# Optimization experiments

Measured on AMD Instinct MI355X. Metric: run time of the kernel, lower is better.

## Reference

```python
import jax, jax.numpy as jnp
import numpy as np
import math

B, S, D, H = 4, 1024, 1024, 16
Dh = D // H
THETA = 10000.0
LAMBDA_INIT = 0.8  # current_lambda_init_for_scaling (no set_lambda_init_for_scaling call)
GN_EPS = 1e-5


def setup_inputs() -> dict:
    key = jax.random.key(0)
    ks = jax.random.split(key, 14)
    w = 0.02
    return {
        "x_norm": jax.random.normal(ks[0], (B, S, D), jnp.float32),
        "learned_lambda": jax.random.uniform(ks[1], (), jnp.float32),
        "hierarchical_mask_C": jax.random.uniform(ks[2], (1, 1, S, S), jnp.float32),
        "padding_mask": jnp.ones((B, S), jnp.int32),
        "wq_w": jax.random.normal(ks[3], (2 * D, D), jnp.float32) * w,
        "wq_b": jnp.zeros((2 * D,), jnp.float32),
        "wk_w": jax.random.normal(ks[4], (2 * D, D), jnp.float32) * w,
        "wk_b": jnp.zeros((2 * D,), jnp.float32),
        "wv_w": jax.random.normal(ks[5], (D, D), jnp.float32) * w,
        "wv_b": jnp.zeros((D,), jnp.float32),
        "out_w": jax.random.normal(ks[6], (D, D), jnp.float32) * w,
        "out_b": jnp.zeros((D,), jnp.float32),
        "gn_w": jnp.ones((D,), jnp.float32),
        "gn_b": jnp.zeros((D,), jnp.float32),
    }


def _rope_tables(seq_len):
    freqs = 1.0 / (THETA ** (jnp.arange(0, Dh, 2, dtype=jnp.float32) / Dh))  # [Dh/2]
    t = jnp.arange(seq_len, dtype=jnp.float32)
    ang = jnp.outer(t, freqs)  # [S, Dh/2]
    return jnp.cos(ang), jnp.sin(ang)


def _apply_rope(x, cos, sin):
    # x: [B,H,S,Dh]; cos/sin: [S,Dh/2] broadcast over B,H
    x1, x2 = x[..., : Dh // 2], x[..., Dh // 2 :]
    return jnp.concatenate((x1 * cos - x2 * sin, x1 * sin + x2 * cos), axis=-1)


def _heads(x):
    # [B,S,D] -> [B,H,S,Dh]
    b, s, _ = x.shape
    return x.reshape(b, s, H, Dh).transpose(0, 2, 1, 3)


def _masked_softmax(q, k, key_pad_bad):
    scores = jnp.einsum("bhqd,bhkd->bhqk", q, k) / math.sqrt(Dh)
    scores = jnp.where(key_pad_bad[:, None, None, :], -1e9, scores)
    return jax.nn.softmax(scores, axis=-1)


def reference(x_norm, learned_lambda, hierarchical_mask_C, padding_mask,
              wq_w, wq_b, wk_w, wk_b, wv_w, wv_b, out_w, out_b, gn_w, gn_b):
    b, s, _ = x_norm.shape
    q_proj = x_norm @ wq_w.T + wq_b  # [B,S,2D]
    k_proj = x_norm @ wk_w.T + wk_b
    v_proj = x_norm @ wv_w.T + wv_b
    q1, q2 = _heads(q_proj[..., :D]), _heads(q_proj[..., D:])
    k1, k2 = _heads(k_proj[..., :D]), _heads(k_proj[..., D:])
    v = _heads(v_proj)

    cos, sin = _rope_tables(s)
    q1, k1 = _apply_rope(q1, cos, sin), _apply_rope(k1, cos, sin)
    q2, k2 = _apply_rope(q2, cos, sin), _apply_rope(k2, cos, sin)

    key_pad_bad = padding_mask == 0  # [B,S]
    a1 = _masked_softmax(q1, k1, key_pad_bad)
    a2 = _masked_softmax(q2, k2, key_pad_bad)
    diff = a1 - learned_lambda * a2
    combined = hierarchical_mask_C * diff  # [B,H,S,S]

    ctx = jnp.einsum("bhqk,bhkd->bhqd", combined, v)  # [B,H,S,Dh]
    merged = ctx.transpose(0, 2, 1, 3).reshape(b, s, D)  # [B,S,D]

    # GroupNorm(n_heads, d_model) applied on [B, D, S]: normalize per (batch, head-group)
    g = merged.reshape(b, s, H, Dh)
    mean = g.mean(axis=(1, 3), keepdims=True)
    var = ((g - mean) ** 2).mean(axis=(1, 3), keepdims=True)
    normed = ((g - mean) * jax.lax.rsqrt(var + GN_EPS)).reshape(b, s, D)
    normed = normed * gn_w + gn_b

    scaled = normed * (1.0 - LAMBDA_INIT)
    output = scaled @ out_w.T + out_b
    return output, a1, a2
```

## Files before the change

kernel.cpp:

```cpp
#include <hip/hip_runtime.h>
#include <hip/hip_bf16.h>
#include <hip/hip_fp16.h>
#include <cstdint>

#define HSZ    4194304ull
#define S_LEN  1024
#define NHEAD  16
#define DH     64

typedef __attribute__((ext_vector_type(8))) short bf16x8;
typedef __attribute__((ext_vector_type(8))) unsigned short u16x8;
typedef __attribute__((ext_vector_type(4))) unsigned short u16x4;
typedef __attribute__((ext_vector_type(4))) float f32x4;
#define MFMA(a,b,c) __builtin_amdgcn_mfma_f32_16x16x32_bf16(a,b,c,0,0,0)

__device__ __forceinline__ unsigned short f2bf(float f) {
    union { float f; uint32_t u; } v; v.f = f;
    uint32_t r = (v.u + 0x7fffu + ((v.u >> 16) & 1u)) >> 16;
    return (unsigned short)r;
}
__device__ __forceinline__ float bf2f(unsigned short u) {
    union { uint32_t u; float f; } v; v.u = (uint32_t)u << 16;
    return v.f;
}
__device__ __forceinline__ unsigned short f2h(float f) { return __half_as_ushort(__float2half(f)); }
__device__ __forceinline__ float h2f(unsigned short u) { return __half2float(__ushort_as_half(u)); }

__device__ __forceinline__ void bar_lds() {
    asm volatile("s_waitcnt lgkmcnt(0)" ::: "memory");
    __builtin_amdgcn_s_barrier();
}

__global__ __launch_bounds__(256) void conv_x_kernel(
    const float* __restrict__ X, unsigned short* __restrict__ xh, unsigned short* __restrict__ xl)
{
    const int idx = blockIdx.x * 256 + threadIdx.x;
    float4 a = *(const float4*)&X[idx * 8];
    float4 b = *(const float4*)&X[idx * 8 + 4];
    float v[8] = {a.x, a.y, a.z, a.w, b.x, b.y, b.z, b.w};
    u16x8 hi, lo;
#pragma unroll
    for (int j = 0; j < 8; ++j) {
        unsigned short h = f2bf(v[j]);
        hi[j] = h;
        lo[j] = f2bf(v[j] - bf2f(h));
    }
    *(u16x8*)&xh[idx * 8] = hi;
    *(u16x8*)&xl[idx * 8] = lo;
}

__global__ __launch_bounds__(256) void conv_w_kernel(
    const float* __restrict__ wq, const float* __restrict__ wk,
    const float* __restrict__ wv, const float* __restrict__ wo,
    unsigned short* __restrict__ Wcat)
{
    const int idx = blockIdx.x * 256 + threadIdx.x;
    const int row = idx >> 7;
    const int cg  = idx & 127;
    const float* src;
    int rl;
    if (row < 2048)      { src = wq; rl = row; }
    else if (row < 4096) { src = wk; rl = row - 2048; }
    else if (row < 5120) { src = wv; rl = row - 4096; }
    else                 { src = wo; rl = row - 5120; }
    float4 a = *(const float4*)&src[(size_t)rl * 1024 + cg * 8];
    float4 b = *(const float4*)&src[(size_t)rl * 1024 + cg * 8 + 4];
    float v[8] = {a.x, a.y, a.z, a.w, b.x, b.y, b.z, b.w};
    u16x8 o;
#pragma unroll
    for (int j = 0; j < 8; ++j) o[j] = f2bf(v[j]);
    *(u16x8*)&Wcat[(size_t)row * 1024 + cg * 8] = o;
}

__global__ __launch_bounds__(256) void conv_c_kernel(
    const float* __restrict__ C, unsigned short* __restrict__ Cb)
{
    const int idx = blockIdx.x * 256 + threadIdx.x;
    float4 a = *(const float4*)&C[idx * 8];
    float4 b = *(const float4*)&C[idx * 8 + 4];
    float v[8] = {a.x, a.y, a.z, a.w, b.x, b.y, b.z, b.w};
    u16x8 o;
#pragma unroll
    for (int j = 0; j < 8; ++j) o[j] = f2bf(v[j]);
    *(u16x8*)&Cb[idx * 8] = o;
}

__global__ __launch_bounds__(256) void proj_mfma_kernel(
    const unsigned short* __restrict__ xh, const unsigned short* __restrict__ xl,
    const unsigned short* __restrict__ Wcat,
    const float* __restrict__ bq, const float* __restrict__ bk, const float* __restrict__ bv,
    unsigned short* __restrict__ qk, unsigned short* __restrict__ vt)
{
    __shared__ __align__(16) unsigned short Ah[128 * 64];
    __shared__ __align__(16) unsigned short Al[128 * 64];
    __shared__ __align__(16) unsigned short Bs[128 * 64];

    const int t   = threadIdx.x;
    const int bid = blockIdx.x;
    const int swz = (bid & 7) * 160 + (bid >> 3);
    const int n_idx = swz % 40, m_idx = swz / 40;
    const int m0 = m_idx * 128, n0 = n_idx * 128;
    const int w = t >> 6, l = t & 63, ln = l & 15, kg = l >> 4;
    const int wm = w >> 1, wn = w & 1;
    const bool useLo = (n0 < 2048);

    f32x4 acc[4][4];
#pragma unroll
    for (int i = 0; i < 4; ++i)
#pragma unroll
        for (int j = 0; j < 4; ++j) acc[i][j] = (f32x4){0.f, 0.f, 0.f, 0.f};

    for (int k0 = 0; k0 < 1024; k0 += 64) {
        __syncthreads();
#pragma unroll
        for (int i = 0; i < 4; ++i) {
            const int e   = t + i * 256;
            const int row = e >> 3, cg = e & 7;
            const int off = (row * 128 + cg * 16) ^ ((row & 7) << 4);
            const size_t ga = (size_t)(m0 + row) * 1024 + k0 + cg * 8;
            const size_t gb = (size_t)(n0 + row) * 1024 + k0 + cg * 8;
            *(bf16x8*)((char*)Ah + off) = *(const bf16x8*)(xh + ga);
            if (useLo)
                *(bf16x8*)((char*)Al + off) = *(const bf16x8*)(xl + ga);
            *(bf16x8*)((char*)Bs + off) = *(const bf16x8*)(Wcat + gb);
        }
        __syncthreads();
#pragma unroll
        for (int ks = 0; ks < 2; ++ks) {
            bf16x8 bfrag[4];
#pragma unroll
            for (int nj = 0; nj < 4; ++nj) {
                const int row = wn * 64 + nj * 16 + ln;
                const int off = (row * 128 + ks * 64 + kg * 16) ^ ((row & 7) << 4);
                bfrag[nj] = *(const bf16x8*)((const char*)Bs + off);
            }
#pragma unroll
            for (int mi = 0; mi < 4; ++mi) {
                const int row = wm * 64 + mi * 16 + ln;
                const int off = (row * 128 + ks * 64 + kg * 16) ^ ((row & 7) << 4);
                bf16x8 ah = *(const bf16x8*)((const char*)Ah + off);
#pragma unroll
                for (int nj = 0; nj < 4; ++nj)
                    acc[mi][nj] = MFMA(ah, bfrag[nj], acc[mi][nj]);
                if (useLo) {
                    bf16x8 al = *(const bf16x8*)((const char*)Al + off);
#pragma unroll
                    for (int nj = 0; nj < 4; ++nj)
                        acc[mi][nj] = MFMA(al, bfrag[nj], acc[mi][nj]);
                }
            }
        }
    }

    const int seg = (n0 < 2048) ? 0 : (n0 < 4096 ? 1 : 2);
    if (seg < 2) {
        const float* bias = (seg == 0) ? bq : bk;
#pragma unroll
        for (int njp = 0; njp < 2; ++njp) {
            const int n1  = n0 + wn * 64 + njp * 16 + ln;
            const int nl1 = n1 - seg * 2048;
            const int head = (nl1 >> 6) & 15;
            const int dd   = nl1 & 63;
            const float bb1 = bias[nl1];
            const float bb2 = bias[nl1 + 32];
            const float freq = exp2f((float)dd * (-13.287712379549449f / 32.0f));
            unsigned short* hiT;
            unsigned short* loT = nullptr;
            if (seg == 0) {
                const int tq = (nl1 >> 10);
                hiT = qk + (size_t)(tq * 2)     * HSZ;
                loT = qk + (size_t)(tq * 2 + 1) * HSZ;
            } else {
                hiT = qk + (size_t)(4 + (nl1 >> 10)) * HSZ;
            }
#pragma unroll
            for (int mi = 0; mi < 4; ++mi) {
                const int mb = m0 + wm * 64 + mi * 16 + kg * 4;
#pragma unroll
                for (int r = 0; r < 4; ++r) {
                    const int m = mb + r, b_ = m >> 10, s = m & 1023;
                    float sn, cs;
                    sincosf((float)s * freq, &sn, &cs);
                    const float x1 = acc[mi][njp][r]     + bb1;
                    const float x2 = acc[mi][njp + 2][r] + bb2;
                    const float r1 = x1 * cs - x2 * sn;
                    const float r2 = x1 * sn + x2 * cs;
                    const size_t base = (((size_t)(b_ * 16 + head)) * 1024 + s) * 64;
                    const unsigned short h1 = f2bf(r1), h2 = f2bf(r2);
                    hiT[base + dd]      = h1;
                    hiT[base + dd + 32] = h2;
                    if (seg == 0) {
                        loT[base + dd]      = f2bf(r1 - bf2f(h1));
                        loT[base + dd + 32] = f2bf(r2 - bf2f(h2));
                    }
                }
            }
        }
    } else {
#pragma unroll
        for (int mi = 0; mi < 4; ++mi) {
#pragma unroll
            for (int nj = 0; nj < 4; ++nj) {
                const int n  = n0 + wn * 64 + nj * 16 + ln;
                const int nl = n - 4096;
                const float bb = bv[nl];
                const int head = nl >> 6, d = nl & 63;
                const int mb = m0 + wm * 64 + mi * 16 + kg * 4;
                const int b = mb >> 10, sb = mb & 1023;
                u16x4 o;
#pragma unroll
                for (int r = 0; r < 4; ++r) o[r] = f2bf(acc[mi][nj][r] + bb);
                *(u16x4*)(vt + ((size_t)(b * 16 + head) * 64 + d) * 1024 + sb) = o;
            }
        }
    }
}

__global__ __launch_bounds__(512, 4) void attn_kernel(
    const unsigned short* __restrict__ qk,
    const unsigned short* __restrict__ vt,
    const unsigned short* __restrict__ Cb,
    const int* __restrict__ pad,
    const float* __restrict__ lam_p,
    float* __restrict__ out_a1, float* __restrict__ out_a2,
    float* __restrict__ merged)
{
    __shared__ __align__(16) unsigned short sc[16][1032];
    __shared__ __align__(16) float pmax[16][8];
    __shared__ __align__(16) f32x4 red[256];

    const int t  = threadIdx.x;
    const int w  = t >> 6;
    const int l  = t & 63;
    const int ln = l & 15;
    const int g  = l >> 4;
    const int kf = g * 8;

    const int flat = blockIdx.x;
    const int virt = (flat & 7) * 512 + (flat >> 3);
    const int bh = virt >> 6, b = bh >> 4, h = bh & 15;
    const int q0 = (virt & 63) * 16;
    const float lam = lam_p[0];

    const f32x4 Z = {0.f, 0.f, 0.f, 0.f};
    f32x4 ctx = Z;
    const int dt  = w & 3;
    const int khf = w >> 2;

    uint32_t padm = 0;
#pragma unroll
    for (int j = 0; j < 8; ++j)
        padm |= (pad[b * S_LEN + w * 128 + j * 16 + ln] != 0 ? 1u : 0u) << j;

    for (int p = 0; p < 2; ++p) {
        const unsigned short* Qh = qk + (size_t)(2*p)     * HSZ + (size_t)bh * 65536;
        const unsigned short* Ql = qk + (size_t)(2*p + 1) * HSZ + (size_t)bh * 65536;
        const unsigned short* K  = qk + (size_t)(4 + p)   * HSZ + (size_t)bh * 65536;

        const size_t qb = (size_t)(q0 + ln) * 64 + kf;
        const bf16x8 qh0 = *(const bf16x8*)(Qh + qb);
        const bf16x8 qh1 = *(const bf16x8*)(Qh + qb + 32);
        const bf16x8 ql0 = *(const bf16x8*)(Ql + qb);
        const bf16x8 ql1 = *(const bf16x8*)(Ql + qb + 32);

        bar_lds();

        f32x4 m = {-3.4e38f, -3.4e38f, -3.4e38f, -3.4e38f};
#pragma unroll 2
        for (int j = 0; j < 8; ++j) {
            const int key = w * 128 + j * 16 + ln;
            const size_t kb = (size_t)key * 64 + kf;
            const bf16x8 k0 = *(const bf16x8*)(K + kb);
            const bf16x8 k1 = *(const bf16x8*)(K + kb + 32);
            f32x4 a = Z;
            a = MFMA(qh0, k0, a); a = MFMA(qh1, k1, a);
            a = MFMA(ql0, k0, a); a = MFMA(ql1, k1, a);
            const bool ok = (padm >> j) & 1;
            const float mm = ok ? 0.125f : 0.0f;
            const float ma = ok ? 0.0f : -60000.0f;
#pragma unroll
            for (int r = 0; r < 4; ++r) {
                const float sv = a[r] * mm + ma;
                m[r] = fmaxf(m[r], sv);
                sc[g * 4 + r][key] = f2h(sv);
            }
        }
#pragma unroll
        for (int off = 1; off < 16; off <<= 1)
#pragma unroll
            for (int r = 0; r < 4; ++r) m[r] = fmaxf(m[r], __shfl_xor(m[r], off));
        if (ln == 0) {
#pragma unroll
            for (int r = 0; r < 4; ++r) pmax[g * 4 + r][w] = m[r];
        }
        bar_lds();

        {
            const int row = t >> 5, ci = t & 31;
            float fm = -3.4e38f;
#pragma unroll
            for (int wi = 0; wi < 8; ++wi) fm = fmaxf(fm, pmax[row][wi]);
            float sum = 0.f;
#pragma unroll 2
            for (int it = 0; it < 4; ++it) {
                const int c0 = ci * 8 + it * 256;
                const u16x8 xv = *(const u16x8*)&sc[row][c0];
                u16x8 ev;
#pragma unroll
                for (int i = 0; i < 8; ++i) {
                    const float ee = __expf(h2f(xv[i]) - fm);
                    sum += ee;
                    ev[i] = f2h(ee);
                }
                *(u16x8*)&sc[row][c0] = ev;
            }
#pragma unroll
            for (int off = 1; off < 32; off <<= 1) sum += __shfl_xor(sum, off);
            const float inv = 1.0f / sum;
            const float fac = p ? -lam : 1.0f;
            float* aout = (p ? out_a2 : out_a1) + ((size_t)bh * S_LEN + q0 + row) * S_LEN;
            const unsigned short* Crow = Cb + (size_t)(q0 + row) * S_LEN;
#pragma unroll 2
            for (int it = 0; it < 4; ++it) {
                const int c0 = ci * 8 + it * 256;
                const u16x8 ev = *(const u16x8*)&sc[row][c0];
                const u16x8 cv = *(const u16x8*)&Crow[c0];
                float av[8];
#pragma unroll
                for (int i = 0; i < 8; ++i) av[i] = h2f(ev[i]) * inv;
                f32x4 oa = {av[0], av[1], av[2], av[3]};
                f32x4 ob = {av[4], av[5], av[6], av[7]};
                __builtin_nontemporal_store(oa, (f32x4*)&aout[c0]);
                __builtin_nontemporal_store(ob, (f32x4*)&aout[c0 + 4]);
                u16x8 cw;
#pragma unroll
                for (int i = 0; i < 8; ++i) cw[i] = f2bf(bf2f(cv[i]) * av[i] * fac);
                *(u16x8*)&sc[row][c0] = cw;
            }
        }
        bar_lds();

        {
            const unsigned short* vtb = vt + (size_t)bh * 65536
                                           + (size_t)(dt * 16 + ln) * S_LEN + kf;
#pragma unroll 4
            for (int ks = 0; ks < 16; ++ks) {
                const int kk = khf * 16 + ks;
                const bf16x8 A0 = *(const bf16x8*)&sc[ln][kk * 32 + kf];
                const bf16x8 Bv = *(const bf16x8*)(vtb + kk * 32);
                ctx = MFMA(A0, Bv, ctx);
            }
        }
    }

    __syncthreads();
    if (khf == 1) red[dt * 64 + l] = ctx;
    __syncthreads();
    if (khf == 0) {
        ctx += red[dt * 64 + l];
        const int col = h * DH + dt * 16 + ln;
#pragma unroll
        for (int r = 0; r < 4; ++r)
            merged[(size_t)(b * S_LEN + q0 + g * 4 + r) * 1024 + col] = ctx[r];
    }
}

__global__ __launch_bounds__(256) void stats_kernel(
    const float* __restrict__ merged, float* __restrict__ stats)
{
    const int g = blockIdx.x;
    const int b = g >> 4, h = g & 15;
    const int t = threadIdx.x;
    float sum = 0.f, sq = 0.f;
    for (int i = t; i < 65536; i += 256) {
        const int s = i >> 6, d = i & 63;
        const float v = merged[((size_t)(b * S_LEN + s)) * 1024 + h * DH + d];
        sum += v; sq += v * v;
    }
#pragma unroll
    for (int off = 32; off > 0; off >>= 1) {
        sum += __shfl_xor(sum, off);
        sq  += __shfl_xor(sq, off);
    }
    __shared__ float rs[4], rq[4];
    const int wid = t >> 6;
    if ((t & 63) == 0) { rs[wid] = sum; rq[wid] = sq; }
    __syncthreads();
    if (t == 0) {
        const float S = rs[0] + rs[1] + rs[2] + rs[3];
        const float Q = rq[0] + rq[1] + rq[2] + rq[3];
        const float mean = S * (1.0f / 65536.0f);
        const float var  = Q * (1.0f / 65536.0f) - mean * mean;
        stats[2*g]   = mean;
        stats[2*g+1] = rsqrtf(var + 1e-5f);
    }
}

__global__ __launch_bounds__(256) void norm_conv_kernel(
    const float* __restrict__ merged, const float* __restrict__ stats,
    const float* __restrict__ gw, const float* __restrict__ gb,
    unsigned short* __restrict__ normed)
{
    const int idx = blockIdx.x * 256 + threadIdx.x;
    const int m = idx >> 7;
    const int col8 = (idx & 127) * 8;
    const int b = m >> 10, h = col8 >> 6;
    const float mean = stats[2 * (b * 16 + h)];
    const float inv  = stats[2 * (b * 16 + h) + 1];
    float4 v0 = *(const float4*)&merged[(size_t)m * 1024 + col8];
    float4 v1 = *(const float4*)&merged[(size_t)m * 1024 + col8 + 4];
    float4 w0 = *(const float4*)&gw[col8];
    float4 w1 = *(const float4*)&gw[col8 + 4];
    float4 g0 = *(const float4*)&gb[col8];
    float4 g1 = *(const float4*)&gb[col8 + 4];
    float v[8] = {v0.x, v0.y, v0.z, v0.w, v1.x, v1.y, v1.z, v1.w};
    float wv[8] = {w0.x, w0.y, w0.z, w0.w, w1.x, w1.y, w1.z, w1.w};
    float gv[8] = {g0.x, g0.y, g0.z, g0.w, g1.x, g1.y, g1.z, g1.w};
    u16x8 o;
#pragma unroll
    for (int j = 0; j < 8; ++j)
        o[j] = f2bf(((v[j] - mean) * inv * wv[j] + gv[j]) * 0.2f);
    *(u16x8*)&normed[(size_t)m * 1024 + col8] = o;
}

__global__ __launch_bounds__(256) void out_mfma_kernel(
    const unsigned short* __restrict__ An, const unsigned short* __restrict__ Wo_bf,
    const float* __restrict__ bo, float* __restrict__ out)
{
    __shared__ __align__(16) unsigned short As[128 * 64];
    __shared__ __align__(16) unsigned short Bs[128 * 64];

    const int t   = threadIdx.x;
    const int bid = blockIdx.x;
    const int swz = (bid & 7) * 32 + (bid >> 3);
    const int n_idx = swz & 7, m_idx = swz >> 3;
    const int m0 = m_idx * 128, n0 = n_idx * 128;
    const int w = t >> 6, l = t & 63, ln = l & 15, kg = l >> 4;
    const int wm = w >> 1, wn = w & 1;

    f32x4 acc[4][4];
#pragma unroll
    for (int i = 0; i < 4; ++i)
#pragma unroll
        for (int j = 0; j < 4; ++j) acc[i][j] = (f32x4){0.f, 0.f, 0.f, 0.f};

    for (int k0 = 0; k0 < 1024; k0 += 64) {
        __syncthreads();
#pragma unroll
        for (int i = 0; i < 4; ++i) {
            const int e   = t + i * 256;
            const int row = e >> 3, cg = e & 7;
            const int off = (row * 128 + cg * 16) ^ ((row & 7) << 4);
            *(bf16x8*)((char*)As + off) = *(const bf16x8*)(An + (size_t)(m0 + row) * 1024 + k0 + cg * 8);
            *(bf16x8*)((char*)Bs + off) = *(const bf16x8*)(Wo_bf + (size_t)(n0 + row) * 1024 + k0 + cg * 8);
        }
        __syncthreads();
#pragma unroll
        for (int ks = 0; ks < 2; ++ks) {
            bf16x8 bfrag[4];
#pragma unroll
            for (int nj = 0; nj < 4; ++nj) {
                const int row = wn * 64 + nj * 16 + ln;
                const int off = (row * 128 + ks * 64 + kg * 16) ^ ((row & 7) << 4);
                bfrag[nj] = *(const bf16x8*)((const char*)Bs + off);
            }
#pragma unroll
            for (int mi = 0; mi < 4; ++mi) {
                const int row = wm * 64 + mi * 16 + ln;
                const int off = (row * 128 + ks * 64 + kg * 16) ^ ((row & 7) << 4);
                bf16x8 af = *(const bf16x8*)((const char*)As + off);
#pragma unroll
                for (int nj = 0; nj < 4; ++nj)
                    acc[mi][nj] = MFMA(af, bfrag[nj], acc[mi][nj]);
            }
        }
    }

#pragma unroll
    for (int mi = 0; mi < 4; ++mi) {
#pragma unroll
        for (int nj = 0; nj < 4; ++nj) {
            const int n = n0 + wn * 64 + nj * 16 + ln;
            const float bb = bo[n];
            const int mb = m0 + wm * 64 + mi * 16 + kg * 4;
#pragma unroll
            for (int r = 0; r < 4; ++r)
                out[(size_t)(mb + r) * 1024 + n] = acc[mi][nj][r] + bb;
        }
    }
}

extern "C" void kernel_launch(void* const* d_in, const int* in_sizes, int n_in,
                              void* d_out, int out_size, void* d_ws, size_t ws_size,
                              hipStream_t stream)
{
    const float* x   = (const float*)d_in[0];
    const float* lam = (const float*)d_in[1];
    const float* C   = (const float*)d_in[2];
    const int*   pad = (const int*)  d_in[3];
    const float* wq  = (const float*)d_in[4];
    const float* bq  = (const float*)d_in[5];
    const float* wk  = (const float*)d_in[6];
    const float* bk  = (const float*)d_in[7];
    const float* wv  = (const float*)d_in[8];
    const float* bv  = (const float*)d_in[9];
    const float* wo  = (const float*)d_in[10];
    const float* bo  = (const float*)d_in[11];
    const float* gw  = (const float*)d_in[12];
    const float* gb  = (const float*)d_in[13];

    float* out = (float*)d_out;
    float* a1  = out + 4194304;
    float* a2  = a1 + 67108864;

    unsigned short* xh   = (unsigned short*)d_ws;
    unsigned short* xl   = xh + HSZ;
    unsigned short* qk   = xl + HSZ;
    unsigned short* vt   = qk + 6 * HSZ;
    unsigned short* Wcat = vt + HSZ;
    float* merged        = (float*)(Wcat + 6144ull * 1024);
    float* stats         = merged + HSZ;
    unsigned short* normed = (unsigned short*)(stats + 128);
    unsigned short* Cb   = xh;

    conv_x_kernel<<<2048, 256, 0, stream>>>(x, xh, xl);
    conv_w_kernel<<<3072, 256, 0, stream>>>(wq, wk, wv, wo, Wcat);
    proj_mfma_kernel<<<1280, 256, 0, stream>>>(xh, xl, Wcat, bq, bk, bv, qk, vt);
    conv_c_kernel<<<512, 256, 0, stream>>>(C, Cb);
    attn_kernel<<<4096, 512, 0, stream>>>(qk, vt, Cb, pad, lam, a1, a2, merged);
    stats_kernel<<<64, 256, 0, stream>>>(merged, stats);
    norm_conv_kernel<<<2048, 256, 0, stream>>>(merged, stats, gw, gb, normed);
    out_mfma_kernel<<<256, 256, 0, stream>>>(normed, Wcat + 5120ull * 1024, bo, out);
}
```

Before: 584.6 us.

## Fuse both softmax branches into one pass and single PV matmul

```diff
diff --git a/kernel.cpp b/kernel.cpp
--- a/kernel.cpp
+++ b/kernel.cpp
@@ -225,8 +225,10 @@
     float* __restrict__ out_a1, float* __restrict__ out_a2,
     float* __restrict__ merged)
 {
-    __shared__ __align__(16) unsigned short sc[16][1032];
-    __shared__ __align__(16) float pmax[16][8];
+    __shared__ __align__(16) unsigned short sc1[16][1032];
+    __shared__ __align__(16) unsigned short sc2[16][1032];
+    __shared__ __align__(16) float pmax1[16][8];
+    __shared__ __align__(16) float pmax2[16][8];
     __shared__ __align__(16) f32x4 red[256];
 
     const int t  = threadIdx.x;
@@ -252,104 +254,156 @@
     for (int j = 0; j < 8; ++j)
         padm |= (pad[b * S_LEN + w * 128 + j * 16 + ln] != 0 ? 1u : 0u) << j;
 
-    for (int p = 0; p < 2; ++p) {
-        const unsigned short* Qh = qk + (size_t)(2*p)     * HSZ + (size_t)bh * 65536;
-        const unsigned short* Ql = qk + (size_t)(2*p + 1) * HSZ + (size_t)bh * 65536;
-        const unsigned short* K  = qk + (size_t)(4 + p)   * HSZ + (size_t)bh * 65536;
-
-        const size_t qb = (size_t)(q0 + ln) * 64 + kf;
-        const bf16x8 qh0 = *(const bf16x8*)(Qh + qb);
-        const bf16x8 qh1 = *(const bf16x8*)(Qh + qb + 32);
-        const bf16x8 ql0 = *(const bf16x8*)(Ql + qb);
-        const bf16x8 ql1 = *(const bf16x8*)(Ql + qb + 32);
-
-        bar_lds();
-
-        f32x4 m = {-3.4e38f, -3.4e38f, -3.4e38f, -3.4e38f};
+    const unsigned short* Q1h = qk + (size_t)0 * HSZ + (size_t)bh * 65536;
+    const unsigned short* Q1l = qk + (size_t)1 * HSZ + (size_t)bh * 65536;
+    const unsigned short* Q2h = qk + (size_t)2 * HSZ + (size_t)bh * 65536;
+    const unsigned short* Q2l = qk + (size_t)3 * HSZ + (size_t)bh * 65536;
+    const unsigned short* K1  = qk + (size_t)4 * HSZ + (size_t)bh * 65536;
+    const unsigned short* K2  = qk + (size_t)5 * HSZ + (size_t)bh * 65536;
+
+    const size_t qb = (size_t)(q0 + ln) * 64 + kf;
+    const bf16x8 q1h0 = *(const bf16x8*)(Q1h + qb);
+    const bf16x8 q1h1 = *(const bf16x8*)(Q1h + qb + 32);
+    const bf16x8 q1l0 = *(const bf16x8*)(Q1l + qb);
+    const bf16x8 q1l1 = *(const bf16x8*)(Q1l + qb + 32);
+    const bf16x8 q2h0 = *(const bf16x8*)(Q2h + qb);
+    const bf16x8 q2h1 = *(const bf16x8*)(Q2h + qb + 32);
+    const bf16x8 q2l0 = *(const bf16x8*)(Q2l + qb);
+    const bf16x8 q2l1 = *(const bf16x8*)(Q2l + qb + 32);
+
+    {
+        f32x4 m1 = {-3.4e38f, -3.4e38f, -3.4e38f, -3.4e38f};
 #pragma unroll 2
         for (int j = 0; j < 8; ++j) {
             const int key = w * 128 + j * 16 + ln;
             const size_t kb = (size_t)key * 64 + kf;
-            const bf16x8 k0 = *(const bf16x8*)(K + kb);
-            const bf16x8 k1 = *(const bf16x8*)(K + kb + 32);
+            const bf16x8 k0 = *(const bf16x8*)(K1 + kb);
+            const bf16x8 k1 = *(const bf16x8*)(K1 + kb + 32);
             f32x4 a = Z;
-            a = MFMA(qh0, k0, a); a = MFMA(qh1, k1, a);
-            a = MFMA(ql0, k0, a); a = MFMA(ql1, k1, a);
+            a = MFMA(q1h0, k0, a); a = MFMA(q1h1, k1, a);
+            a = MFMA(q1l0, k0, a); a = MFMA(q1l1, k1, a);
             const bool ok = (padm >> j) & 1;
             const float mm = ok ? 0.125f : 0.0f;
             const float ma = ok ? 0.0f : -60000.0f;
 #pragma unroll
             for (int r = 0; r < 4; ++r) {
                 const float sv = a[r] * mm + ma;
-                m[r] = fmaxf(m[r], sv);
-                sc[g * 4 + r][key] = f2h(sv);
+                m1[r] = fmaxf(m1[r], sv);
+                sc1[g * 4 + r][key] = f2h(sv);
             }
         }
 #pragma unroll
         for (int off = 1; off < 16; off <<= 1)
 #pragma unroll
-            for (int r = 0; r < 4; ++r) m[r] = fmaxf(m[r], __shfl_xor(m[r], off));
+            for (int r = 0; r < 4; ++r) m1[r] = fmaxf(m1[r], __shfl_xor(m1[r], off));
         if (ln == 0) {
 #pragma unroll
-            for (int r = 0; r < 4; ++r) pmax[g * 4 + r][w] = m[r];
-        }
-        bar_lds();
-
-        {
-            const int row = t >> 5, ci = t & 31;
-            float fm = -3.4e38f;
-#pragma unroll
-            for (int wi = 0; wi < 8; ++wi) fm = fmaxf(fm, pmax[row][wi]);
-            float sum = 0.f;
+            for (int r = 0; r < 4; ++r) pmax1[g * 4 + r][w] = m1[r];
+        }
+        f32x4 m2 = {-3.4e38f, -3.4e38f, -3.4e38f, -3.4e38f};
 #pragma unroll 2
-            for (int it = 0; it < 4; ++it) {
-                const int c0 = ci * 8 + it * 256;
-                const u16x8 xv = *(const u16x8*)&sc[row][c0];
-                u16x8 ev;
-#pragma unroll
-                for (int i = 0; i < 8; ++i) {
-                    const float ee = __expf(h2f(xv[i]) - fm);
-                    sum += ee;
-                    ev[i] = f2h(ee);
-                }
-                *(u16x8*)&sc[row][c0] = ev;
-            }
-#pragma unroll
-            for (int off = 1; off < 32; off <<= 1) sum += __shfl_xor(sum, off);
-            const float inv = 1.0f / sum;
-            const float fac = p ? -lam : 1.0f;
-            float* aout = (p ? out_a2 : out_a1) + ((size_t)bh * S_LEN + q0 + row) * S_LEN;
-            const unsigned short* Crow = Cb + (size_t)(q0 + row) * S_LEN;
+        for (int j = 0; j < 8; ++j) {
+            const int key = w * 128 + j * 16 + ln;
+            const size_t kb = (size_t)key * 64 + kf;
+            const bf16x8 k0 = *(const bf16x8*)(K2 + kb);
+            const bf16x8 k1 = *(const bf16x8*)(K2 + kb + 32);
+            f32x4 a = Z;
+            a = MFMA(q2h0, k0, a); a = MFMA(q2h1, k1, a);
+            a = MFMA(q2l0, k0, a); a = MFMA(q2l1, k1, a);
+            const bool ok = (padm >> j) & 1;
+            const float mm = ok ? 0.125f : 0.0f;
+            const float ma = ok ? 0.0f : -60000.0f;
+#pragma unroll
+            for (int r = 0; r < 4; ++r) {
+                const float sv = a[r] * mm + ma;
+                m2[r] = fmaxf(m2[r], sv);
+                sc2[g * 4 + r][key] = f2h(sv);
+            }
+        }
+#pragma unroll
+        for (int off = 1; off < 16; off <<= 1)
+#pragma unroll
+            for (int r = 0; r < 4; ++r) m2[r] = fmaxf(m2[r], __shfl_xor(m2[r], off));
+        if (ln == 0) {
+#pragma unroll
+            for (int r = 0; r < 4; ++r) pmax2[g * 4 + r][w] = m2[r];
+        }
+    }
+    bar_lds();
+
+    {
+        const int row = t >> 5, ci = t & 31;
+        float fm1 = -3.4e38f, fm2 = -3.4e38f;
+#pragma unroll
+        for (int wi = 0; wi < 8; ++wi) {
+            fm1 = fmaxf(fm1, pmax1[row][wi]);
+            fm2 = fmaxf(fm2, pmax2[row][wi]);
+        }
+        float sum1 = 0.f, sum2 = 0.f;
 #pragma unroll 2
-            for (int it = 0; it < 4; ++it) {
-                const int c0 = ci * 8 + it * 256;
-                const u16x8 ev = *(const u16x8*)&sc[row][c0];
-                const u16x8 cv = *(const u16x8*)&Crow[c0];
-                float av[8];
-#pragma unroll
-                for (int i = 0; i < 8; ++i) av[i] = h2f(ev[i]) * inv;
-                f32x4 oa = {av[0], av[1], av[2], av[3]};
-                f32x4 ob = {av[4], av[5], av[6], av[7]};
-                __builtin_nontemporal_store(oa, (f32x4*)&aout[c0]);
-                __builtin_nontemporal_store(ob, (f32x4*)&aout[c0 + 4]);
-                u16x8 cw;
-#pragma unroll
-                for (int i = 0; i < 8; ++i) cw[i] = f2bf(bf2f(cv[i]) * av[i] * fac);
-                *(u16x8*)&sc[row][c0] = cw;
-            }
-        }
-        bar_lds();
-
-        {
-            const unsigned short* vtb = vt + (size_t)bh * 65536
-                                           + (size_t)(dt * 16 + ln) * S_LEN + kf;
+        for (int it = 0; it < 4; ++it) {
+            const int c0 = ci * 8 + it * 256;
+            const u16x8 xv1 = *(const u16x8*)&sc1[row][c0];
+            const u16x8 xv2 = *(const u16x8*)&sc2[row][c0];
+            u16x8 ev1, ev2;
+#pragma unroll
+            for (int i = 0; i < 8; ++i) {
+                const float e1 = __expf(h2f(xv1[i]) - fm1);
+                const float e2 = __expf(h2f(xv2[i]) - fm2);
+                sum1 += e1; sum2 += e2;
+                ev1[i] = f2h(e1); ev2[i] = f2h(e2);
+            }
+            *(u16x8*)&sc1[row][c0] = ev1;
+            *(u16x8*)&sc2[row][c0] = ev2;
+        }
+#pragma unroll
+        for (int off = 1; off < 32; off <<= 1) {
+            sum1 += __shfl_xor(sum1, off);
+            sum2 += __shfl_xor(sum2, off);
+        }
+        const float inv1 = 1.0f / sum1;
+        const float inv2 = 1.0f / sum2;
+        float* aout1 = out_a1 + ((size_t)bh * S_LEN + q0 + row) * S_LEN;
+        float* aout2 = out_a2 + ((size_t)bh * S_LEN + q0 + row) * S_LEN;
+        const unsigned short* Crow = Cb + (size_t)(q0 + row) * S_LEN;
+#pragma unroll 2
+        for (int it = 0; it < 4; ++it) {
+            const int c0 = ci * 8 + it * 256;
+            const u16x8 ev1 = *(const u16x8*)&sc1[row][c0];
+            const u16x8 ev2 = *(const u16x8*)&sc2[row][c0];
+            const u16x8 cv  = *(const u16x8*)&Crow[c0];
+            float av1[8], av2[8];
+#pragma unroll
+            for (int i = 0; i < 8; ++i) {
+                av1[i] = h2f(ev1[i]) * inv1;
+                av2[i] = h2f(ev2[i]) * inv2;
+            }
+            f32x4 oa1 = {av1[0], av1[1], av1[2], av1[3]};
+            f32x4 ob1 = {av1[4], av1[5], av1[6], av1[7]};
+            f32x4 oa2 = {av2[0], av2[1], av2[2], av2[3]};
+            f32x4 ob2 = {av2[4], av2[5], av2[6], av2[7]};
+            __builtin_nontemporal_store(oa1, (f32x4*)&aout1[c0]);
+            __builtin_nontemporal_store(ob1, (f32x4*)&aout1[c0 + 4]);
+            __builtin_nontemporal_store(oa2, (f32x4*)&aout2[c0]);
+            __builtin_nontemporal_store(ob2, (f32x4*)&aout2[c0 + 4]);
+            u16x8 cw;
+#pragma unroll
+            for (int i = 0; i < 8; ++i)
+                cw[i] = f2bf(bf2f(cv[i]) * (av1[i] - lam * av2[i]));
+            *(u16x8*)&sc1[row][c0] = cw;
+        }
+    }
+    bar_lds();
+
+    {
+        const unsigned short* vtb = vt + (size_t)bh * 65536
+                                       + (size_t)(dt * 16 + ln) * S_LEN + kf;
 #pragma unroll 4
-            for (int ks = 0; ks < 16; ++ks) {
-                const int kk = khf * 16 + ks;
-                const bf16x8 A0 = *(const bf16x8*)&sc[ln][kk * 32 + kf];
-                const bf16x8 Bv = *(const bf16x8*)(vtb + kk * 32);
-                ctx = MFMA(A0, Bv, ctx);
-            }
+        for (int ks = 0; ks < 16; ++ks) {
+            const int kk = khf * 16 + ks;
+            const bf16x8 A0 = *(const bf16x8*)&sc1[ln][kk * 32 + kf];
+            const bf16x8 Bv = *(const bf16x8*)(vtb + kk * 32);
+            ctx = MFMA(A0, Bv, ctx);
         }
     }
 
```

After: 527.9 us, median of 2. 9.7% less time.
